# Optimization experiments

Hardware: AMD Instinct MI355X
Metric: run time of the kernel (lower is better)

Reference implementation:

```python
import jax, jax.numpy as jnp
import numpy as np

N, F_IN, HID, OUT, K, L = 16000, 16, 256, 128, 8, 3


def setup_inputs() -> dict:
    key = jax.random.key(0)
    ks = jax.random.split(key, 8)
    rn = lambda k, sh, sc: (jax.random.normal(k, sh, jnp.float32) * sc)
    return {
        "x": rn(ks[0], (N, F_IN), 1.0),
        "coords": rn(ks[1], (N, 3), 1.0),
        "We": rn(ks[2], (F_IN, HID), 0.1),
        "be": jnp.zeros((HID,), jnp.float32),
        "gnn_W": rn(ks[3], (L, HID, HID), 0.05),
        "gnn_b": jnp.zeros((L, HID), jnp.float32),
        "Wp1": rn(ks[4], (HID, HID // 2), 0.05),
        "bp1": jnp.zeros((HID // 2,), jnp.float32),
        "Wp2": rn(ks[5], (HID // 2, OUT), 0.05),
        "bp2": jnp.zeros((OUT,), jnp.float32),
    }


def knn_edges(coords, k=K):
    # squared pairwise distances (same ordering as torch.cdist) -> kNN, drop self
    sq = jnp.sum(coords * coords, axis=1)
    d2 = sq[:, None] + sq[None, :] - 2.0 * (coords @ coords.T)  # [N, N]
    _, idx = jax.lax.top_k(-d2, k + 1)            # smallest k+1 (incl. self)
    nbr = idx[:, 1:]                               # [N, k]
    src = jnp.broadcast_to(jnp.arange(coords.shape[0])[:, None], nbr.shape)
    return src.reshape(-1), nbr.reshape(-1)       # edge_index rows


def gcn_layer(h, W, b, src, dst, n):
    # GCN with added self-loops and symmetric degree normalization
    deg = jnp.ones((n,), h.dtype).at[dst].add(1.0)   # in-degree + self-loop
    norm = jax.lax.rsqrt(deg)
    hw = h @ W                                        # [N, HID]
    msg = hw[src] * (norm[src] * norm[dst])[:, None]  # gather + scale
    agg = jax.ops.segment_sum(msg, dst, num_segments=n)
    agg = agg + hw * (norm * norm)[:, None]           # self-loop term
    return agg + b


def reference(x, coords, We, be, gnn_W, gnn_b, Wp1, bp1, Wp2, bp2):
    n = x.shape[0]
    src, dst = knn_edges(coords)
    h = x @ We + be                     # survey encoder -> [N, HID]
    for i in range(L):
        h = gcn_layer(h, gnn_W[i], gnn_b[i], src, dst, n)
        h = jax.nn.relu(h)              # dropout is identity in eval mode
    g = jnp.mean(h, axis=0)             # mean pooling (batch=None) -> [HID]
    out = jax.nn.relu(g @ Wp1 + bp1) @ Wp2 + bp2  # output projection -> [OUT]
    return out
```

## Files before the change

### kernel.cpp

```cpp
#include <hip/hip_runtime.h>
#include <math.h>

#define N_NODES 16000
#define F_IN    16
#define HID     256
#define OUTD    128
#define KNN     8
#define LAYERS  3
#define NEDGE   (N_NODES * KNN)

#define NPAD    16384
#define PARTS   4
#define PART_SZ (NPAD / PARTS)
#define SEGS    32
#define NMIN    (PARTS * SEGS)
#define CAPP    32

typedef __attribute__((ext_vector_type(8))) short  s8v;
typedef __attribute__((ext_vector_type(4))) float  f4v;

__device__ __forceinline__ unsigned short f2bf(float x) {
    unsigned u = __float_as_uint(x);
    unsigned r = u + 0x7fffu + ((u >> 16) & 1u);
    return (unsigned short)(r >> 16);
}
__device__ __forceinline__ float bf2f(unsigned short b) {
    return __uint_as_float(((unsigned)b) << 16);
}

__global__ __launch_bounds__(256) void prep_kernel(const float* __restrict__ coords,
                                                   float4* __restrict__ cand) {
    int i = blockIdx.x * 256 + threadIdx.x;
    if (i >= NPAD) return;
    if (i < N_NODES) {
        float x = coords[3 * i], y = coords[3 * i + 1], z = coords[3 * i + 2];
        cand[i] = make_float4(-2.f * x, -2.f * y, -2.f * z, x * x + y * y + z * z);
    } else {
        cand[i] = make_float4(0.f, 0.f, 0.f, INFINITY);
    }
}

#define DIST(qx, qy, qz, c) fmaf(qx, c.x, fmaf(qy, c.y, fmaf(qz, c.z, c.w)))

__global__ __launch_bounds__(256) void knn_min_kernel(const float* __restrict__ coords,
                                                      const float4* __restrict__ cand,
                                                      float* __restrict__ minv) {
    int tid  = threadIdx.x;
    int seg  = tid & 31;
    int qg   = tid >> 5;
    int qbase = blockIdx.x * 64;
    int part = blockIdx.y;

    float qx[8], qy[8], qz[8], m[8];
#pragma unroll
    for (int i = 0; i < 8; ++i) {
        int q = qbase + i * 8 + qg;
        qx[i] = coords[q * 3]; qy[i] = coords[q * 3 + 1]; qz[i] = coords[q * 3 + 2];
        m[i] = INFINITY;
    }

    int pbase = part * PART_SZ;
#pragma unroll 2
    for (int c0 = 0; c0 < PART_SZ; c0 += 128) {
        float4 v0 = cand[pbase + c0 + seg];
        float4 v1 = cand[pbase + c0 + seg + 32];
        float4 v2 = cand[pbase + c0 + seg + 64];
        float4 v3 = cand[pbase + c0 + seg + 96];
#pragma unroll
        for (int i = 0; i < 8; ++i) {
            float d0 = DIST(qx[i], qy[i], qz[i], v0);
            float d1 = DIST(qx[i], qy[i], qz[i], v1);
            float d2 = DIST(qx[i], qy[i], qz[i], v2);
            float d3 = DIST(qx[i], qy[i], qz[i], v3);
            m[i] = fminf(m[i], fminf(fminf(d0, d1), fminf(d2, d3)));
        }
    }
#pragma unroll
    for (int i = 0; i < 8; ++i) {
        int q = qbase + i * 8 + qg;
        minv[(q * PARTS + part) * SEGS + seg] = m[i];
    }
}

__global__ __launch_bounds__(256) void tau_kernel(const float* __restrict__ minv,
                                                  float* __restrict__ tau) {
    int q = blockIdx.x * 256 + threadIdx.x;
    if (q >= N_NODES) return;
    float b[9];
#pragma unroll
    for (int p = 0; p < 9; ++p) b[p] = INFINITY;
    const float4* mv = (const float4*)(minv + (size_t)q * NMIN);
#pragma unroll
    for (int c = 0; c < 16; ++c) {
        float4 a0 = mv[c * 2], a1 = mv[c * 2 + 1];
        float v = fminf(fminf(fminf(a0.x, a0.y), fminf(a0.z, a0.w)),
                        fminf(fminf(a1.x, a1.y), fminf(a1.z, a1.w)));
#pragma unroll
        for (int p = 8; p >= 1; --p) {
            bool  up = v < b[p - 1];
            float nd = up ? b[p - 1] : (v < b[p] ? v : b[p]);
            b[p] = nd;
        }
        if (v < b[0]) b[0] = v;
    }
    tau[q] = b[8];
}

__global__ __launch_bounds__(256) void knn_collect_kernel(const float* __restrict__ coords,
                                                          const float4* __restrict__ cand,
                                                          const float* __restrict__ tau,
                                                          int* __restrict__ cnt,
                                                          float2* __restrict__ cl) {
    __shared__ int scnt[64];
    int tid  = threadIdx.x;
    int seg  = tid & 31;
    int qg   = tid >> 5;
    int qbase = blockIdx.x * 64;
    int part  = blockIdx.y;

    float qx[8], qy[8], qz[8], tt[8];
#pragma unroll
    for (int i = 0; i < 8; ++i) {
        int q = qbase + i * 8 + qg;
        qx[i] = coords[q * 3]; qy[i] = coords[q * 3 + 1]; qz[i] = coords[q * 3 + 2];
        tt[i] = tau[q];
    }
    if (tid < 64) scnt[tid] = 0;
    __syncthreads();

    int pbase = part * PART_SZ;
    for (int c0 = 0; c0 < PART_SZ; c0 += 128) {
        float4 v0 = cand[pbase + c0 + seg];
        float4 v1 = cand[pbase + c0 + seg + 32];
        float4 v2 = cand[pbase + c0 + seg + 64];
        float4 v3 = cand[pbase + c0 + seg + 96];
        int jb = pbase + c0 + seg;
#pragma unroll
        for (int i = 0; i < 8; ++i) {
            float d0 = DIST(qx[i], qy[i], qz[i], v0);
            float d1 = DIST(qx[i], qy[i], qz[i], v1);
            float d2 = DIST(qx[i], qy[i], qz[i], v2);
            float d3 = DIST(qx[i], qy[i], qz[i], v3);
            float m4 = fminf(fminf(d0, d1), fminf(d2, d3));
            if (m4 <= tt[i]) {
                int qi = qbase + i * 8 + qg;
                int cb = (int)(((size_t)qi * PARTS + part) * CAPP);
                if (d0 <= tt[i]) {
                    int pos = atomicAdd(&scnt[i * 8 + qg], 1);
                    if (pos < CAPP) cl[cb + pos] = make_float2(d0, __int_as_float(jb));
                }
                if (d1 <= tt[i]) {
                    int pos = atomicAdd(&scnt[i * 8 + qg], 1);
                    if (pos < CAPP) cl[cb + pos] = make_float2(d1, __int_as_float(jb + 32));
                }
                if (d2 <= tt[i]) {
                    int pos = atomicAdd(&scnt[i * 8 + qg], 1);
                    if (pos < CAPP) cl[cb + pos] = make_float2(d2, __int_as_float(jb + 64));
                }
                if (d3 <= tt[i]) {
                    int pos = atomicAdd(&scnt[i * 8 + qg], 1);
                    if (pos < CAPP) cl[cb + pos] = make_float2(d3, __int_as_float(jb + 96));
                }
            }
        }
    }
    __syncthreads();
    if (tid < 64) cnt[(size_t)(qbase + tid) * PARTS + part] = scnt[tid];
}

#define INS9L(bd, bi, d, j)                                                   \
    {                                                                         \
        _Pragma("unroll")                                                     \
        for (int p = 8; p >= 1; --p) {                                        \
            bool up = (d) < bd[p-1] || ((d) == bd[p-1] && (j) < bi[p-1]);     \
            bool in = (d) < bd[p]   || ((d) == bd[p]   && (j) < bi[p]);       \
            float nd = up ? bd[p-1] : (in ? (d) : bd[p]);                     \
            int   ni = up ? bi[p-1] : (in ? (j) : bi[p]);                     \
            bd[p] = nd; bi[p] = ni;                                           \
        }                                                                     \
        if ((d) < bd[0] || ((d) == bd[0] && (j) < bi[0])) {                   \
            bd[0] = (d); bi[0] = (j);                                         \
        }                                                                     \
    }

__global__ __launch_bounds__(256) void knn_select_kernel(const float* __restrict__ coords,
                                                         const float4* __restrict__ cand,
                                                         const float2* __restrict__ cl,
                                                         const int* __restrict__ cnt,
                                                         int* __restrict__ nbr,
                                                         int* __restrict__ indeg) {
    int q = blockIdx.x * 256 + threadIdx.x;
    if (q >= N_NODES) return;
    float bd[9]; int bi[9];
#pragma unroll
    for (int p = 0; p < 9; ++p) { bd[p] = INFINITY; bi[p] = 0x7fffffff; }
    int n0 = cnt[(size_t)q * PARTS + 0];
    int n1 = cnt[(size_t)q * PARTS + 1];
    int n2 = cnt[(size_t)q * PARTS + 2];
    int n3 = cnt[(size_t)q * PARTS + 3];
    if (n0 <= CAPP && n1 <= CAPP && n2 <= CAPP && n3 <= CAPP) {
#pragma unroll
        for (int p = 0; p < PARTS; ++p) {
            int n = (p == 0) ? n0 : (p == 1) ? n1 : (p == 2) ? n2 : n3;
            const float2* segp = cl + ((size_t)q * PARTS + p) * CAPP;
            for (int i = 0; i < n; ++i) {
                float2 e = segp[i];
                float d = e.x; int j = __float_as_int(e.y);
                INS9L(bd, bi, d, j);
            }
        }
    } else {
        float qx = coords[q*3], qy = coords[q*3+1], qz = coords[q*3+2];
        for (int j = 0; j < NPAD; ++j) {
            float4 c = cand[j];
            float d = DIST(qx, qy, qz, c);
            if (d < bd[8] || (d == bd[8] && j < bi[8])) INS9L(bd, bi, d, j);
        }
    }
#pragma unroll
    for (int p = 1; p < 9; ++p) {
        nbr[q * 8 + p - 1] = bi[p];
        atomicAdd(&indeg[bi[p]], 1);
    }
}

__global__ __launch_bounds__(1024) void scan_kernel(const int* __restrict__ indeg,
                                                    int* __restrict__ offs,
                                                    float* __restrict__ norm) {
    __shared__ int ssum[1024];
    int t = threadIdx.x;
    const int CH = 16;
    int base = t * CH;
    int s = 0;
    for (int c = 0; c < CH; ++c) {
        int idx = base + c;
        if (idx < N_NODES) s += indeg[idx];
    }
    ssum[t] = s;
    __syncthreads();
    for (int d = 1; d < 1024; d <<= 1) {
        int v = (t >= d) ? ssum[t - d] : 0;
        __syncthreads();
        ssum[t] += v;
        __syncthreads();
    }
    int run = ssum[t] - s;
    for (int c = 0; c < CH; ++c) {
        int idx = base + c;
        if (idx < N_NODES) {
            int dg = indeg[idx];
            offs[idx] = run;
            run += dg;
            norm[idx] = rsqrtf((float)(1 + dg));
        }
    }
    if (t == 1023) offs[N_NODES] = ssum[1023];
}

__global__ void fill_kernel(const int* __restrict__ nbr, const int* __restrict__ offs,
                            int* __restrict__ cursor, int* __restrict__ adj) {
    int e = blockIdx.x * blockDim.x + threadIdx.x;
    if (e < NEDGE) {
        int d   = nbr[e];
        int src = e >> 3;
        int pos = atomicAdd(&cursor[d], 1);
        adj[offs[d] + pos] = src;
    }
}

__global__ __launch_bounds__(256) void gemm_kernel(const float* __restrict__ A,
                                                   const float* __restrict__ B,
                                                   float* __restrict__ C,
                                                   int K,
                                                   const float* __restrict__ rowscale,
                                                   const float* __restrict__ bias) {
    __shared__ float As[16][68];
    __shared__ float Bs[16][64];
    int tid = threadIdx.x;
    int rowBase = blockIdx.x * 64;
    int colBase = blockIdx.y * 64;
    int rg = tid >> 4;
    int cg = tid & 15;

    int ar = tid >> 2;
    int ac = (tid & 3) * 4;
    int bk = tid >> 4;
    int bn = (tid & 15) * 4;

    float4 acc0 = {0,0,0,0}, acc1 = {0,0,0,0}, acc2 = {0,0,0,0}, acc3 = {0,0,0,0};

    for (int kb = 0; kb < K; kb += 16) {
        float4 av = *(const float4*)(A + (size_t)(rowBase + ar) * K + kb + ac);
        float4 bv = *(const float4*)(B + (size_t)(kb + bk) * HID + colBase + bn);
        __syncthreads();
        As[ac + 0][ar] = av.x; As[ac + 1][ar] = av.y;
        As[ac + 2][ar] = av.z; As[ac + 3][ar] = av.w;
        *(float4*)&Bs[bk][bn] = bv;
        __syncthreads();
#pragma unroll
        for (int k = 0; k < 16; ++k) {
            float4 a = *(const float4*)&As[k][rg * 4];
            float4 b = *(const float4*)&Bs[k][cg * 4];
            acc0.x = fmaf(a.x, b.x, acc0.x); acc0.y = fmaf(a.x, b.y, acc0.y);
            acc0.z = fmaf(a.x, b.z, acc0.z); acc0.w = fmaf(a.x, b.w, acc0.w);
            acc1.x = fmaf(a.y, b.x, acc1.x); acc1.y = fmaf(a.y, b.y, acc1.y);
            acc1.z = fmaf(a.y, b.z, acc1.z); acc1.w = fmaf(a.y, b.w, acc1.w);
            acc2.x = fmaf(a.z, b.x, acc2.x); acc2.y = fmaf(a.z, b.y, acc2.y);
            acc2.z = fmaf(a.z, b.z, acc2.z); acc2.w = fmaf(a.z, b.w, acc2.w);
            acc3.x = fmaf(a.w, b.x, acc3.x); acc3.y = fmaf(a.w, b.y, acc3.y);
            acc3.z = fmaf(a.w, b.z, acc3.z); acc3.w = fmaf(a.w, b.w, acc3.w);
        }
        __syncthreads();
    }

    int row = rowBase + rg * 4;
    int col = colBase + cg * 4;
    float s0 = 1.f, s1 = 1.f, s2 = 1.f, s3 = 1.f;
    if (rowscale) { s0 = rowscale[row]; s1 = rowscale[row + 1];
                    s2 = rowscale[row + 2]; s3 = rowscale[row + 3]; }
    float4 bb = {0,0,0,0};
    if (bias) bb = *(const float4*)(bias + col);

    float4 v;
    v.x = acc0.x * s0 + bb.x; v.y = acc0.y * s0 + bb.y;
    v.z = acc0.z * s0 + bb.z; v.w = acc0.w * s0 + bb.w;
    *(float4*)(C + (size_t)(row + 0) * HID + col) = v;
    v.x = acc1.x * s1 + bb.x; v.y = acc1.y * s1 + bb.y;
    v.z = acc1.z * s1 + bb.z; v.w = acc1.w * s1 + bb.w;
    *(float4*)(C + (size_t)(row + 1) * HID + col) = v;
    v.x = acc2.x * s2 + bb.x; v.y = acc2.y * s2 + bb.y;
    v.z = acc2.z * s2 + bb.z; v.w = acc2.w * s2 + bb.w;
    *(float4*)(C + (size_t)(row + 2) * HID + col) = v;
    v.x = acc3.x * s3 + bb.x; v.y = acc3.y * s3 + bb.y;
    v.z = acc3.z * s3 + bb.z; v.w = acc3.w * s3 + bb.w;
    *(float4*)(C + (size_t)(row + 3) * HID + col) = v;
}

__global__ __launch_bounds__(256) void wsplit_kernel(const float* __restrict__ W,
                                                     unsigned short* __restrict__ WThi,
                                                     unsigned short* __restrict__ WTlo) {
    int idx = blockIdx.x * 256 + threadIdx.x;
    int l = idx >> 16;
    int r = idx & 65535;
    int k = r >> 8, j = r & 255;
    float x = W[idx];
    unsigned short hb = f2bf(x);
    float hf = bf2f(hb);
    size_t o = (size_t)l * 65536 + j * 256 + k;
    WThi[o] = hb;
    WTlo[o] = f2bf(x - hf);
}

__global__ __launch_bounds__(256) void mfma_gemm_kernel(const float* __restrict__ A,
                                                        const unsigned short* __restrict__ WThi,
                                                        const unsigned short* __restrict__ WTlo,
                                                        unsigned short* __restrict__ C,
                                                        const float* __restrict__ rowscale) {
    __shared__ unsigned short Ahi[64][40], Alo[64][40];
    __shared__ unsigned short Bhi[128][40], Blo[128][40];
    int tid = threadIdx.x;
    int rowBase = blockIdx.x * 64;
    int colBase = blockIdx.y * 128;
    int wave = tid >> 6;
    int lane = tid & 63;
    int fr = lane & 15;
    int fg = lane >> 4;

    int asr = tid >> 2;
    int ask = (tid & 3) * 8;
    int bsj = tid >> 1;
    int bsk = (tid & 1) * 16;

    f4v acc[8];
#pragma unroll
    for (int c = 0; c < 8; ++c) acc[c] = (f4v){0.f, 0.f, 0.f, 0.f};

    for (int kb = 0; kb < HID; kb += 32) {
        const float4* ap = (const float4*)(A + (size_t)(rowBase + asr) * HID + kb + ask);
        float4 a0 = ap[0], a1 = ap[1];
        const uint4* bhp = (const uint4*)(WThi + (size_t)(colBase + bsj) * HID + kb + bsk);
        const uint4* blp = (const uint4*)(WTlo + (size_t)(colBase + bsj) * HID + kb + bsk);
        uint4 bh0 = bhp[0], bh1 = bhp[1];
        uint4 bl0 = blp[0], bl1 = blp[1];

        __syncthreads();
        {
            float xv[8] = {a0.x, a0.y, a0.z, a0.w, a1.x, a1.y, a1.z, a1.w};
            s8v hv, lv;
#pragma unroll
            for (int e = 0; e < 8; ++e) {
                unsigned short hb = f2bf(xv[e]);
                float hf = bf2f(hb);
                hv[e] = (short)hb;
                lv[e] = (short)f2bf(xv[e] - hf);
            }
            *(s8v*)&Ahi[asr][ask] = hv;
            *(s8v*)&Alo[asr][ask] = lv;
        }
        *(uint4*)&Bhi[bsj][bsk]      = bh0;
        *(uint4*)&Bhi[bsj][bsk + 8]  = bh1;
        *(uint4*)&Blo[bsj][bsk]      = bl0;
        *(uint4*)&Blo[bsj][bsk + 8]  = bl1;
        __syncthreads();

        s8v afh = *(s8v*)&Ahi[wave * 16 + fr][fg * 8];
        s8v afl = *(s8v*)&Alo[wave * 16 + fr][fg * 8];
#pragma unroll
        for (int c = 0; c < 8; ++c) {
            s8v bfh = *(s8v*)&Bhi[c * 16 + fr][fg * 8];
            s8v bfl = *(s8v*)&Blo[c * 16 + fr][fg * 8];
            acc[c] = __builtin_amdgcn_mfma_f32_16x16x32_bf16(afh, bfh, acc[c], 0, 0, 0);
            acc[c] = __builtin_amdgcn_mfma_f32_16x16x32_bf16(afh, bfl, acc[c], 0, 0, 0);
            acc[c] = __builtin_amdgcn_mfma_f32_16x16x32_bf16(afl, bfh, acc[c], 0, 0, 0);
        }
    }

    float sc[4];
#pragma unroll
    for (int r = 0; r < 4; ++r) sc[r] = rowscale[rowBase + wave * 16 + fg * 4 + r];
#pragma unroll
    for (int c = 0; c < 8; ++c) {
        int col = colBase + c * 16 + fr;
#pragma unroll
        for (int r = 0; r < 4; ++r) {
            int row = rowBase + wave * 16 + fg * 4 + r;
            C[(size_t)row * HID + col] = f2bf(acc[c][r] * sc[r]);
        }
    }
}

__global__ __launch_bounds__(256) void agg_kernel(const unsigned short* __restrict__ u,
                                                  const float* __restrict__ norm,
                                                  const float* __restrict__ bias,
                                                  const int* __restrict__ offs,
                                                  const int* __restrict__ adj,
                                                  float* __restrict__ hout) {
    int node = blockIdx.x * 4 + (threadIdx.x >> 6);
    int lane = threadIdx.x & 63;
    const ushort4* up = (const ushort4*)u;
    ushort4 sv = up[(size_t)node * 64 + lane];
    float ax = bf2f(sv.x), ay = bf2f(sv.y), az = bf2f(sv.z), aw = bf2f(sv.w);
    int e0 = offs[node], e1 = offs[node + 1];
    for (int e = e0; e < e1; ++e) {
        int s = adj[e];
        ushort4 v = up[(size_t)s * 64 + lane];
        ax += bf2f(v.x); ay += bf2f(v.y); az += bf2f(v.z); aw += bf2f(v.w);
    }
    float nm = norm[node];
    float4 bb = ((const float4*)bias)[lane];
    float4 r;
    r.x = fmaxf(fmaf(nm, ax, bb.x), 0.0f);
    r.y = fmaxf(fmaf(nm, ay, bb.y), 0.0f);
    r.z = fmaxf(fmaf(nm, az, bb.z), 0.0f);
    r.w = fmaxf(fmaf(nm, aw, bb.w), 0.0f);
    ((float4*)hout)[(size_t)node * 64 + lane] = r;
}

__global__ __launch_bounds__(256) void pool_kernel(const float* __restrict__ h,
                                                   float* __restrict__ gsum) {
    int t = threadIdx.x;
    float acc = 0.f;
    int start = blockIdx.x * 250;
    for (int i = 0; i < 250; ++i) acc += h[(size_t)(start + i) * HID + t];
    atomicAdd(&gsum[t], acc);
}

__global__ __launch_bounds__(128) void head_kernel(const float* __restrict__ gsum,
                                                   const float* __restrict__ Wp1,
                                                   const float* __restrict__ bp1,
                                                   const float* __restrict__ Wp2,
                                                   const float* __restrict__ bp2,
                                                   float* __restrict__ out) {
    __shared__ float gl[256];
    __shared__ float hid[128];
    int t = threadIdx.x;
    const float inv = 1.0f / 16000.0f;
    gl[t]       = gsum[t]       * inv;
    gl[t + 128] = gsum[t + 128] * inv;
    __syncthreads();
    float a = bp1[t];
    for (int k = 0; k < 256; ++k) a = fmaf(gl[k], Wp1[k * 128 + t], a);
    hid[t] = fmaxf(a, 0.0f);
    __syncthreads();
    float o = bp2[t];
    for (int k = 0; k < 128; ++k) o = fmaf(hid[k], Wp2[k * 128 + t], o);
    out[t] = o;
}

extern "C" void kernel_launch(void* const* d_in, const int* in_sizes, int n_in,
                              void* d_out, int out_size, void* d_ws, size_t ws_size,
                              hipStream_t stream) {
    const float* x      = (const float*)d_in[0];
    const float* coords = (const float*)d_in[1];
    const float* We     = (const float*)d_in[2];
    const float* be     = (const float*)d_in[3];
    const float* gnn_W  = (const float*)d_in[4];
    const float* gnn_b  = (const float*)d_in[5];
    const float* Wp1    = (const float*)d_in[6];
    const float* bp1    = (const float*)d_in[7];
    const float* Wp2    = (const float*)d_in[8];
    const float* bp2    = (const float*)d_in[9];
    float* out = (float*)d_out;

    char* ws = (char*)d_ws;
    float* h     = (float*)(ws + 0);
    char*  ureg  = ws + 16384000;
    int*   nbr   = (int*)  (ws + 32768000);
    int*   adj   = (int*)  (ws + 33280000);
    int*   indeg = (int*)  (ws + 33792000);
    int*   cursor= (int*)  (ws + 33856000);
    float* gsum  = (float*)(ws + 33920000);
    int*   offs  = (int*)  (ws + 33921024);
    float* norm  = (float*)(ws + 33985152);
    float4* cand = (float4*)(ws + 34049280);

    unsigned short* u16 = (unsigned short*)ureg;
    float*  minv = (float*)ureg;
    float*  tau  = (float*)(ureg + 8192000);
    int*    cnt  = (int*)  (ureg + 8256000);
    unsigned short* WThi = (unsigned short*)(ureg + 8512000);
    unsigned short* WTlo = (unsigned short*)(ureg + 8905216);
    float2* cl   = (float2*)h;

    (void)hipMemsetAsync(ws + 33792000, 0, 129024, stream);

    prep_kernel<<<NPAD / 256, 256, 0, stream>>>(coords, cand);
    knn_min_kernel<<<dim3(N_NODES / 64, PARTS), 256, 0, stream>>>(coords, cand, minv);
    tau_kernel<<<(N_NODES + 255) / 256, 256, 0, stream>>>(minv, tau);
    knn_collect_kernel<<<dim3(N_NODES / 64, PARTS), 256, 0, stream>>>(coords, cand, tau, cnt, cl);
    knn_select_kernel<<<(N_NODES + 255) / 256, 256, 0, stream>>>(coords, cand, cl, cnt, nbr, indeg);

    scan_kernel<<<1, 1024, 0, stream>>>(indeg, offs, norm);
    fill_kernel<<<(NEDGE + 255) / 256, 256, 0, stream>>>(nbr, offs, cursor, adj);

    wsplit_kernel<<<LAYERS * 256, 256, 0, stream>>>(gnn_W, WThi, WTlo);

    dim3 g1(N_NODES / 64, HID / 64);
    gemm_kernel<<<g1, 256, 0, stream>>>(x, We, h, F_IN, nullptr, be);
    for (int l = 0; l < LAYERS; ++l) {
        mfma_gemm_kernel<<<dim3(N_NODES / 64, 2), 256, 0, stream>>>(
            h, WThi + (size_t)l * 65536, WTlo + (size_t)l * 65536, u16, norm);
        agg_kernel<<<N_NODES / 4, 256, 0, stream>>>(u16, norm, gnn_b + (size_t)l * HID,
                                                    offs, adj, h);
    }
    pool_kernel<<<64, 256, 0, stream>>>(h, gsum);
    head_kernel<<<1, 128, 0, stream>>>(gsum, Wp1, bp1, Wp2, bp2, out);
}
```

Measured before the change: 294.9 us.

## Fold small kernels into neighbours and narrow MFMA GEMM column tiles

Removes the memset by zeroing the indeg/cursor region in prep_kernel, folds the tau top-9 reduction into knn_collect_kernel through shared memory, and merges the weight bf16 split into the encoder gemm_kernel as an extra grid row. Separately, the MFMA GEMM tile shrinks from 128 to 64 columns, doubling the block count. The aim is fewer launches and better occupancy. The cost is that each of the four collect partitions recomputes tau redundantly and the MFMA GEMM reloads the A tile twice as often.

```diff
diff --git a/kernel.cpp b/kernel.cpp
--- a/kernel.cpp
+++ b/kernel.cpp
@@ -15,6 +15,7 @@
 #define SEGS    32
 #define NMIN    (PARTS * SEGS)
 #define CAPP    32
+#define NZERO   32256
 
 typedef __attribute__((ext_vector_type(8))) short  s8v;
 typedef __attribute__((ext_vector_type(4))) float  f4v;
@@ -29,12 +30,15 @@
 }
 
 __global__ __launch_bounds__(256) void prep_kernel(const float* __restrict__ coords,
-                                                   float4* __restrict__ cand) {
+                                                   float4* __restrict__ cand,
+                                                   int* __restrict__ zero) {
     int i = blockIdx.x * 256 + threadIdx.x;
+    int z = i * 2;
+    if (z < NZERO) { zero[z] = 0; zero[z + 1] = 0; }
     if (i >= NPAD) return;
     if (i < N_NODES) {
-        float x = coords[3 * i], y = coords[3 * i + 1], z = coords[3 * i + 2];
-        cand[i] = make_float4(-2.f * x, -2.f * y, -2.f * z, x * x + y * y + z * z);
+        float x = coords[3 * i], y = coords[3 * i + 1], z2 = coords[3 * i + 2];
+        cand[i] = make_float4(-2.f * x, -2.f * y, -2.f * z2, x * x + y * y + z2 * z2);
     } else {
         cand[i] = make_float4(0.f, 0.f, 0.f, INFINITY);
     }
@@ -82,51 +86,50 @@
     }
 }
 
-__global__ __launch_bounds__(256) void tau_kernel(const float* __restrict__ minv,
-                                                  float* __restrict__ tau) {
-    int q = blockIdx.x * 256 + threadIdx.x;
-    if (q >= N_NODES) return;
-    float b[9];
-#pragma unroll
-    for (int p = 0; p < 9; ++p) b[p] = INFINITY;
-    const float4* mv = (const float4*)(minv + (size_t)q * NMIN);
-#pragma unroll
-    for (int c = 0; c < 16; ++c) {
-        float4 a0 = mv[c * 2], a1 = mv[c * 2 + 1];
-        float v = fminf(fminf(fminf(a0.x, a0.y), fminf(a0.z, a0.w)),
-                        fminf(fminf(a1.x, a1.y), fminf(a1.z, a1.w)));
-#pragma unroll
-        for (int p = 8; p >= 1; --p) {
-            bool  up = v < b[p - 1];
-            float nd = up ? b[p - 1] : (v < b[p] ? v : b[p]);
-            b[p] = nd;
-        }
-        if (v < b[0]) b[0] = v;
-    }
-    tau[q] = b[8];
-}
-
 __global__ __launch_bounds__(256) void knn_collect_kernel(const float* __restrict__ coords,
                                                           const float4* __restrict__ cand,
-                                                          const float* __restrict__ tau,
+                                                          const float* __restrict__ minv,
                                                           int* __restrict__ cnt,
                                                           float2* __restrict__ cl) {
     __shared__ int scnt[64];
+    __shared__ float stau[64];
     int tid  = threadIdx.x;
     int seg  = tid & 31;
     int qg   = tid >> 5;
     int qbase = blockIdx.x * 64;
     int part  = blockIdx.y;
 
+    if (tid < 64) {
+        int q = qbase + tid;
+        const float4* mv = (const float4*)(minv + (size_t)q * NMIN);
+        float b[9];
+#pragma unroll
+        for (int p = 0; p < 9; ++p) b[p] = INFINITY;
+#pragma unroll
+        for (int c = 0; c < 16; ++c) {
+            float4 a0 = mv[c * 2], a1 = mv[c * 2 + 1];
+            float v = fminf(fminf(fminf(a0.x, a0.y), fminf(a0.z, a0.w)),
+                            fminf(fminf(a1.x, a1.y), fminf(a1.z, a1.w)));
+#pragma unroll
+            for (int p = 8; p >= 1; --p) {
+                bool  up = v < b[p - 1];
+                b[p] = up ? b[p - 1] : (v < b[p] ? v : b[p]);
+            }
+            if (v < b[0]) b[0] = v;
+        }
+        stau[tid] = b[8];
+        scnt[tid] = 0;
+    }
+
     float qx[8], qy[8], qz[8], tt[8];
 #pragma unroll
     for (int i = 0; i < 8; ++i) {
         int q = qbase + i * 8 + qg;
         qx[i] = coords[q * 3]; qy[i] = coords[q * 3 + 1]; qz[i] = coords[q * 3 + 2];
-        tt[i] = tau[q];
-    }
-    if (tid < 64) scnt[tid] = 0;
+    }
     __syncthreads();
+#pragma unroll
+    for (int i = 0; i < 8; ++i) tt[i] = stau[i * 8 + qg];
 
     int pbase = part * PART_SZ;
     for (int c0 = 0; c0 < PART_SZ; c0 += 128) {
@@ -272,8 +275,24 @@
                                                    const float* __restrict__ B,
                                                    float* __restrict__ C,
                                                    int K,
-                                                   const float* __restrict__ rowscale,
-                                                   const float* __restrict__ bias) {
+                                                   const float* __restrict__ bias,
+                                                   const float* __restrict__ Wg,
+                                                   unsigned short* __restrict__ WThi,
+                                                   unsigned short* __restrict__ WTlo) {
+    if (blockIdx.y == 4) {
+        for (int idx = blockIdx.x * 256 + threadIdx.x; idx < LAYERS * 65536;
+             idx += 64000) {
+            int l = idx >> 16;
+            int r = idx & 65535;
+            int k = r >> 8, j = r & 255;
+            float xv = Wg[idx];
+            unsigned short hb = f2bf(xv);
+            size_t o = (size_t)l * 65536 + j * 256 + k;
+            WThi[o] = hb;
+            WTlo[o] = f2bf(xv - bf2f(hb));
+        }
+        return;
+    }
     __shared__ float As[16][68];
     __shared__ float Bs[16][64];
     int tid = threadIdx.x;
@@ -315,40 +334,17 @@
 
     int row = rowBase + rg * 4;
     int col = colBase + cg * 4;
-    float s0 = 1.f, s1 = 1.f, s2 = 1.f, s3 = 1.f;
-    if (rowscale) { s0 = rowscale[row]; s1 = rowscale[row + 1];
-                    s2 = rowscale[row + 2]; s3 = rowscale[row + 3]; }
-    float4 bb = {0,0,0,0};
-    if (bias) bb = *(const float4*)(bias + col);
+    float4 bb = *(const float4*)(bias + col);
 
     float4 v;
-    v.x = acc0.x * s0 + bb.x; v.y = acc0.y * s0 + bb.y;
-    v.z = acc0.z * s0 + bb.z; v.w = acc0.w * s0 + bb.w;
+    v.x = acc0.x + bb.x; v.y = acc0.y + bb.y; v.z = acc0.z + bb.z; v.w = acc0.w + bb.w;
     *(float4*)(C + (size_t)(row + 0) * HID + col) = v;
-    v.x = acc1.x * s1 + bb.x; v.y = acc1.y * s1 + bb.y;
-    v.z = acc1.z * s1 + bb.z; v.w = acc1.w * s1 + bb.w;
+    v.x = acc1.x + bb.x; v.y = acc1.y + bb.y; v.z = acc1.z + bb.z; v.w = acc1.w + bb.w;
     *(float4*)(C + (size_t)(row + 1) * HID + col) = v;
-    v.x = acc2.x * s2 + bb.x; v.y = acc2.y * s2 + bb.y;
-    v.z = acc2.z * s2 + bb.z; v.w = acc2.w * s2 + bb.w;
+    v.x = acc2.x + bb.x; v.y = acc2.y + bb.y; v.z = acc2.z + bb.z; v.w = acc2.w + bb.w;
     *(float4*)(C + (size_t)(row + 2) * HID + col) = v;
-    v.x = acc3.x * s3 + bb.x; v.y = acc3.y * s3 + bb.y;
-    v.z = acc3.z * s3 + bb.z; v.w = acc3.w * s3 + bb.w;
+    v.x = acc3.x + bb.x; v.y = acc3.y + bb.y; v.z = acc3.z + bb.z; v.w = acc3.w + bb.w;
     *(float4*)(C + (size_t)(row + 3) * HID + col) = v;
-}
-
-__global__ __launch_bounds__(256) void wsplit_kernel(const float* __restrict__ W,
-                                                     unsigned short* __restrict__ WThi,
-                                                     unsigned short* __restrict__ WTlo) {
-    int idx = blockIdx.x * 256 + threadIdx.x;
-    int l = idx >> 16;
-    int r = idx & 65535;
-    int k = r >> 8, j = r & 255;
-    float x = W[idx];
-    unsigned short hb = f2bf(x);
-    float hf = bf2f(hb);
-    size_t o = (size_t)l * 65536 + j * 256 + k;
-    WThi[o] = hb;
-    WTlo[o] = f2bf(x - hf);
 }
 
 __global__ __launch_bounds__(256) void mfma_gemm_kernel(const float* __restrict__ A,
@@ -357,10 +353,10 @@
                                                         unsigned short* __restrict__ C,
                                                         const float* __restrict__ rowscale) {
     __shared__ unsigned short Ahi[64][40], Alo[64][40];
-    __shared__ unsigned short Bhi[128][40], Blo[128][40];
+    __shared__ unsigned short Bhi[64][40], Blo[64][40];
     int tid = threadIdx.x;
     int rowBase = blockIdx.x * 64;
-    int colBase = blockIdx.y * 128;
+    int colBase = blockIdx.y * 64;
     int wave = tid >> 6;
     int lane = tid & 63;
     int fr = lane & 15;
@@ -368,20 +364,18 @@
 
     int asr = tid >> 2;
     int ask = (tid & 3) * 8;
-    int bsj = tid >> 1;
-    int bsk = (tid & 1) * 16;
-
-    f4v acc[8];
-#pragma unroll
-    for (int c = 0; c < 8; ++c) acc[c] = (f4v){0.f, 0.f, 0.f, 0.f};
+    int bsj = tid >> 2;
+    int bsk = (tid & 3) * 8;
+
+    f4v acc[4];
+#pragma unroll
+    for (int c = 0; c < 4; ++c) acc[c] = (f4v){0.f, 0.f, 0.f, 0.f};
 
     for (int kb = 0; kb < HID; kb += 32) {
         const float4* ap = (const float4*)(A + (size_t)(rowBase + asr) * HID + kb + ask);
         float4 a0 = ap[0], a1 = ap[1];
-        const uint4* bhp = (const uint4*)(WThi + (size_t)(colBase + bsj) * HID + kb + bsk);
-        const uint4* blp = (const uint4*)(WTlo + (size_t)(colBase + bsj) * HID + kb + bsk);
-        uint4 bh0 = bhp[0], bh1 = bhp[1];
-        uint4 bl0 = blp[0], bl1 = blp[1];
+        uint4 bh0 = *(const uint4*)(WThi + (size_t)(colBase + bsj) * HID + kb + bsk);
+        uint4 bl0 = *(const uint4*)(WTlo + (size_t)(colBase + bsj) * HID + kb + bsk);
 
         __syncthreads();
         {
@@ -397,16 +391,14 @@
             *(s8v*)&Ahi[asr][ask] = hv;
             *(s8v*)&Alo[asr][ask] = lv;
         }
-        *(uint4*)&Bhi[bsj][bsk]      = bh0;
-        *(uint4*)&Bhi[bsj][bsk + 8]  = bh1;
-        *(uint4*)&Blo[bsj][bsk]      = bl0;
-        *(uint4*)&Blo[bsj][bsk + 8]  = bl1;
+        *(uint4*)&Bhi[bsj][bsk] = bh0;
+        *(uint4*)&Blo[bsj][bsk] = bl0;
         __syncthreads();
 
         s8v afh = *(s8v*)&Ahi[wave * 16 + fr][fg * 8];
         s8v afl = *(s8v*)&Alo[wave * 16 + fr][fg * 8];
 #pragma unroll
-        for (int c = 0; c < 8; ++c) {
+        for (int c = 0; c < 4; ++c) {
             s8v bfh = *(s8v*)&Bhi[c * 16 + fr][fg * 8];
             s8v bfl = *(s8v*)&Blo[c * 16 + fr][fg * 8];
             acc[c] = __builtin_amdgcn_mfma_f32_16x16x32_bf16(afh, bfh, acc[c], 0, 0, 0);
@@ -419,7 +411,7 @@
 #pragma unroll
     for (int r = 0; r < 4; ++r) sc[r] = rowscale[rowBase + wave * 16 + fg * 4 + r];
 #pragma unroll
-    for (int c = 0; c < 8; ++c) {
+    for (int c = 0; c < 4; ++c) {
         int col = colBase + c * 16 + fr;
 #pragma unroll
         for (int r = 0; r < 4; ++r) {
@@ -516,29 +508,23 @@
 
     unsigned short* u16 = (unsigned short*)ureg;
     float*  minv = (float*)ureg;
-    float*  tau  = (float*)(ureg + 8192000);
     int*    cnt  = (int*)  (ureg + 8256000);
     unsigned short* WThi = (unsigned short*)(ureg + 8512000);
     unsigned short* WTlo = (unsigned short*)(ureg + 8905216);
     float2* cl   = (float2*)h;
 
-    (void)hipMemsetAsync(ws + 33792000, 0, 129024, stream);
-
-    prep_kernel<<<NPAD / 256, 256, 0, stream>>>(coords, cand);
+    prep_kernel<<<NPAD / 256, 256, 0, stream>>>(coords, cand, indeg);
     knn_min_kernel<<<dim3(N_NODES / 64, PARTS), 256, 0, stream>>>(coords, cand, minv);
-    tau_kernel<<<(N_NODES + 255) / 256, 256, 0, stream>>>(minv, tau);
-    knn_collect_kernel<<<dim3(N_NODES / 64, PARTS), 256, 0, stream>>>(coords, cand, tau, cnt, cl);
+    knn_collect_kernel<<<dim3(N_NODES / 64, PARTS), 256, 0, stream>>>(coords, cand, minv, cnt, cl);
     knn_select_kernel<<<(N_NODES + 255) / 256, 256, 0, stream>>>(coords, cand, cl, cnt, nbr, indeg);
 
     scan_kernel<<<1, 1024, 0, stream>>>(indeg, offs, norm);
     fill_kernel<<<(NEDGE + 255) / 256, 256, 0, stream>>>(nbr, offs, cursor, adj);
 
-    wsplit_kernel<<<LAYERS * 256, 256, 0, stream>>>(gnn_W, WThi, WTlo);
-
-    dim3 g1(N_NODES / 64, HID / 64);
-    gemm_kernel<<<g1, 256, 0, stream>>>(x, We, h, F_IN, nullptr, be);
+    gemm_kernel<<<dim3(N_NODES / 64, 5), 256, 0, stream>>>(x, We, h, F_IN, be,
+                                                           gnn_W, WThi, WTlo);
     for (int l = 0; l < LAYERS; ++l) {
-        mfma_gemm_kernel<<<dim3(N_NODES / 64, 2), 256, 0, stream>>>(
+        mfma_gemm_kernel<<<dim3(N_NODES / 64, 4), 256, 0, stream>>>(
             h, WThi + (size_t)l * 65536, WTlo + (size_t)l * 65536, u16, norm);
         agg_kernel<<<N_NODES / 4, 256, 0, stream>>>(u16, norm, gnn_b + (size_t)l * HID,
                                                     offs, adj, h);
```

After: 287.4 us. 2.5% less time.
